# Performance work log

Hardware: AMD Instinct MI355X
Metric: run time of the kernel (lower is better)

## Reference

```python
import jax, jax.numpy as jnp
import numpy as np

BN_EPS = 1e-5


def setup_inputs() -> dict:
    key = jax.random.key(0)
    k1, k2 = jax.random.split(key)
    B, Cin, H, W_ = 16, 2048, 64, 64
    Cout = 256
    x = jax.random.normal(k1, (B, Cin, H, W_), dtype=jnp.float32)
    # 1x1 conv weight (bias-free, followed by BN) stored as [Cout, Cin]
    W = jax.random.normal(k2, (Cout, Cin), dtype=jnp.float32) * (1.0 / np.sqrt(Cin))
    gamma = jnp.ones((Cout,), dtype=jnp.float32)
    beta = jnp.zeros((Cout,), dtype=jnp.float32)
    running_mean = jnp.zeros((Cout,), dtype=jnp.float32)
    running_var = jnp.ones((Cout,), dtype=jnp.float32)
    return {"x": x, "W": W, "gamma": gamma, "beta": beta,
            "running_mean": running_mean, "running_var": running_var}


def reference(x, W, gamma, beta, running_mean, running_var):
    B, Cin, H, Wd = x.shape
    # Global average pool -> [B, Cin]
    pooled = jnp.mean(x, axis=(2, 3))
    # 1x1 conv on 1x1 spatial == GEMM: [B, Cin] @ [Cin, Cout] -> [B, Cout]
    y = jnp.einsum('bc,oc->bo', pooled, W)
    # BatchNorm2d in eval mode (running stats), fused scale/shift
    inv_std = jax.lax.rsqrt(running_var + BN_EPS)
    y = (y - running_mean) * (gamma * inv_std) + beta
    # ReLU
    y = jnp.maximum(y, 0.0)
    # Bilinear upsample from 1x1 (align_corners=False) == pure broadcast
    out = jnp.broadcast_to(y[:, :, None, None], (B, y.shape[1], H, Wd))
    return out
```

## Files before the change

kernel.cpp:

```cpp
#include <hip/hip_runtime.h>

#define BN_EPS 1e-5f

__global__ __launch_bounds__(256) void pool_kernel(const float* __restrict__ x,
                                                   float* __restrict__ pooled) {
    const int plane = blockIdx.x;
    const float4* xp = reinterpret_cast<const float4*>(x + (size_t)plane * 4096);
    float s = 0.f;
#pragma unroll
    for (int j = 0; j < 4; ++j) {
        float4 v = xp[threadIdx.x + j * 256];
        s += (v.x + v.y) + (v.z + v.w);
    }
#pragma unroll
    for (int off = 32; off > 0; off >>= 1) s += __shfl_down(s, off, 64);
    __shared__ float wsum[4];
    const int wid = threadIdx.x >> 6;
    const int lane = threadIdx.x & 63;
    if (lane == 0) wsum[wid] = s;
    __syncthreads();
    if (threadIdx.x == 0) {
        float t = (wsum[0] + wsum[1]) + (wsum[2] + wsum[3]);
        pooled[plane] = t * (1.0f / 4096.0f);
    }
}

__global__ __launch_bounds__(256) void gemm_bn_bcast_kernel(
    const float* __restrict__ pooled, const float* __restrict__ Wm,
    const float* __restrict__ gamma, const float* __restrict__ beta,
    const float* __restrict__ rmean, const float* __restrict__ rvar,
    float* __restrict__ out) {
    const int wid = threadIdx.x >> 6;
    const int lane = threadIdx.x & 63;
    const int gw = blockIdx.x * 4 + wid;
    const int b = gw >> 8;
    const int o = gw & 255;

    const float4* pr = reinterpret_cast<const float4*>(pooled + b * 2048);
    const float4* wr = reinterpret_cast<const float4*>(Wm + (size_t)o * 2048);
    float s = 0.f;
#pragma unroll
    for (int k = 0; k < 8; ++k) {
        float4 p = pr[lane + k * 64];
        float4 w = wr[lane + k * 64];
        s += p.x * w.x + p.y * w.y + p.z * w.z + p.w * w.w;
    }
#pragma unroll
    for (int off = 32; off > 0; off >>= 1) s += __shfl_down(s, off, 64);
    float y = __shfl(s, 0, 64);

    const float inv_std = rsqrtf(rvar[o] + BN_EPS);
    y = (y - rmean[o]) * (gamma[o] * inv_std) + beta[o];
    y = fmaxf(y, 0.f);

    float4 v = make_float4(y, y, y, y);
    float4* op = reinterpret_cast<float4*>(out + (size_t)gw * 4096);
#pragma unroll
    for (int j = 0; j < 16; ++j) op[j * 64 + lane] = v;
}

extern "C" void kernel_launch(void* const* d_in, const int* in_sizes, int n_in,
                              void* d_out, int out_size, void* d_ws, size_t ws_size,
                              hipStream_t stream) {
    const float* x     = (const float*)d_in[0];
    const float* Wm    = (const float*)d_in[1];
    const float* gamma = (const float*)d_in[2];
    const float* beta  = (const float*)d_in[3];
    const float* rmean = (const float*)d_in[4];
    const float* rvar  = (const float*)d_in[5];
    float* out = (float*)d_out;

    float* pooled = (float*)d_ws;

    pool_kernel<<<16 * 2048, 256, 0, stream>>>(x, pooled);
    gemm_bn_bcast_kernel<<<4096 / 4, 256, 0, stream>>>(pooled, Wm, gamma, beta,
                                                       rmean, rvar, out);
}
```

Baseline: 111.2 us.

## Fuse pool and GEMM into persistent cooperative kernel with grid sync

```diff
diff --git a/kernel.cpp b/kernel.cpp
--- a/kernel.cpp
+++ b/kernel.cpp
@@ -1,62 +1,92 @@
 #include <hip/hip_runtime.h>
+#include <hip/hip_cooperative_groups.h>
+
+namespace cg = cooperative_groups;
 
 #define BN_EPS 1e-5f
+#define NPLANES (16 * 2048)
+#define NOUT    (16 * 256)
 
-__global__ __launch_bounds__(256) void pool_kernel(const float* __restrict__ x,
-                                                   float* __restrict__ pooled) {
-    const int plane = blockIdx.x;
-    const float4* xp = reinterpret_cast<const float4*>(x + (size_t)plane * 4096);
+typedef float f32x4 __attribute__((ext_vector_type(4)));
+
+__device__ __forceinline__ void pool_plane(const float* __restrict__ x,
+                                           float* __restrict__ pooled,
+                                           int plane, int lane) {
+    const f32x4* xp = reinterpret_cast<const f32x4*>(x + (size_t)plane * 4096);
     float s = 0.f;
 #pragma unroll
-    for (int j = 0; j < 4; ++j) {
-        float4 v = xp[threadIdx.x + j * 256];
+    for (int k = 0; k < 16; ++k) {
+        f32x4 v = __builtin_nontemporal_load(&xp[lane + k * 64]);
         s += (v.x + v.y) + (v.z + v.w);
     }
 #pragma unroll
     for (int off = 32; off > 0; off >>= 1) s += __shfl_down(s, off, 64);
-    __shared__ float wsum[4];
-    const int wid = threadIdx.x >> 6;
-    const int lane = threadIdx.x & 63;
-    if (lane == 0) wsum[wid] = s;
-    __syncthreads();
-    if (threadIdx.x == 0) {
-        float t = (wsum[0] + wsum[1]) + (wsum[2] + wsum[3]);
-        pooled[plane] = t * (1.0f / 4096.0f);
-    }
+    if (lane == 0) pooled[plane] = s * (1.0f / 4096.0f);
 }
 
-__global__ __launch_bounds__(256) void gemm_bn_bcast_kernel(
-    const float* __restrict__ pooled, const float* __restrict__ Wm,
-    const float* __restrict__ gamma, const float* __restrict__ beta,
-    const float* __restrict__ rmean, const float* __restrict__ rvar,
-    float* __restrict__ out) {
-    const int wid = threadIdx.x >> 6;
-    const int lane = threadIdx.x & 63;
-    const int gw = blockIdx.x * 4 + wid;
-    const int b = gw >> 8;
-    const int o = gw & 255;
-
-    const float4* pr = reinterpret_cast<const float4*>(pooled + b * 2048);
-    const float4* wr = reinterpret_cast<const float4*>(Wm + (size_t)o * 2048);
+__device__ __forceinline__ void gemm_bn_bcast(
+    int idx, int lane, const float* __restrict__ pooled,
+    const float* __restrict__ Wm, const float* __restrict__ gamma,
+    const float* __restrict__ beta, const float* __restrict__ rmean,
+    const float* __restrict__ rvar, float* __restrict__ out) {
+    const int b = idx >> 8;
+    const int o = idx & 255;
+    const f32x4* pr = reinterpret_cast<const f32x4*>(pooled + b * 2048);
+    const f32x4* wr = reinterpret_cast<const f32x4*>(Wm + (size_t)o * 2048);
     float s = 0.f;
 #pragma unroll
     for (int k = 0; k < 8; ++k) {
-        float4 p = pr[lane + k * 64];
-        float4 w = wr[lane + k * 64];
+        f32x4 p = pr[lane + k * 64];
+        f32x4 w = wr[lane + k * 64];
         s += p.x * w.x + p.y * w.y + p.z * w.z + p.w * w.w;
     }
 #pragma unroll
     for (int off = 32; off > 0; off >>= 1) s += __shfl_down(s, off, 64);
     float y = __shfl(s, 0, 64);
+    y = (y - rmean[o]) * (gamma[o] * rsqrtf(rvar[o] + BN_EPS)) + beta[o];
+    y = fmaxf(y, 0.f);
+    f32x4 v = {y, y, y, y};
+    f32x4* op = reinterpret_cast<f32x4*>(out + (size_t)idx * 4096);
+#pragma unroll
+    for (int j = 0; j < 16; ++j)
+        __builtin_nontemporal_store(v, &op[j * 64 + lane]);
+}
 
-    const float inv_std = rsqrtf(rvar[o] + BN_EPS);
-    y = (y - rmean[o]) * (gamma[o] * inv_std) + beta[o];
-    y = fmaxf(y, 0.f);
+__global__ __launch_bounds__(256, 4) void fused_kernel(
+    const float* __restrict__ x, const float* __restrict__ Wm,
+    const float* __restrict__ gamma, const float* __restrict__ beta,
+    const float* __restrict__ rmean, const float* __restrict__ rvar,
+    float* __restrict__ pooled, float* __restrict__ out) {
+    const int lane = threadIdx.x & 63;
+    const int gw   = blockIdx.x * 4 + (threadIdx.x >> 6);
+    const int NW   = gridDim.x * 4;
 
-    float4 v = make_float4(y, y, y, y);
-    float4* op = reinterpret_cast<float4*>(out + (size_t)gw * 4096);
-#pragma unroll
-    for (int j = 0; j < 16; ++j) op[j * 64 + lane] = v;
+    for (int plane = gw; plane < NPLANES; plane += NW)
+        pool_plane(x, pooled, plane, lane);
+
+    __threadfence();
+    cg::this_grid().sync();
+    __threadfence();
+
+    for (int idx = gw; idx < NOUT; idx += NW)
+        gemm_bn_bcast(idx, lane, pooled, Wm, gamma, beta, rmean, rvar, out);
+}
+
+__global__ __launch_bounds__(256) void pool_kernel(const float* __restrict__ x,
+                                                   float* __restrict__ pooled) {
+    const int lane = threadIdx.x & 63;
+    const int gw   = blockIdx.x * 4 + (threadIdx.x >> 6);
+    pool_plane(x, pooled, gw, lane);
+}
+
+__global__ __launch_bounds__(256) void gemm_kernel(
+    const float* __restrict__ pooled, const float* __restrict__ Wm,
+    const float* __restrict__ gamma, const float* __restrict__ beta,
+    const float* __restrict__ rmean, const float* __restrict__ rvar,
+    float* __restrict__ out) {
+    const int lane = threadIdx.x & 63;
+    const int gw   = blockIdx.x * 4 + (threadIdx.x >> 6);
+    gemm_bn_bcast(gw, lane, pooled, Wm, gamma, beta, rmean, rvar, out);
 }
 
 extern "C" void kernel_launch(void* const* d_in, const int* in_sizes, int n_in,
@@ -68,11 +98,27 @@
     const float* beta  = (const float*)d_in[3];
     const float* rmean = (const float*)d_in[4];
     const float* rvar  = (const float*)d_in[5];
-    float* out = (float*)d_out;
-
+    float* out    = (float*)d_out;
     float* pooled = (float*)d_ws;
 
-    pool_kernel<<<16 * 2048, 256, 0, stream>>>(x, pooled);
-    gemm_bn_bcast_kernel<<<4096 / 4, 256, 0, stream>>>(pooled, Wm, gamma, beta,
-                                                       rmean, rvar, out);
+    int maxBlocksPerCU = 0;
+    hipError_t qerr = hipOccupancyMaxActiveBlocksPerMultiprocessor(
+        &maxBlocksPerCU, fused_kernel, 256, 0);
+
+    bool launched = false;
+    if (qerr == hipSuccess && maxBlocksPerCU > 0) {
+        int grid = maxBlocksPerCU * 256;
+        if (grid > 1024) grid = 1024;
+        void* args[] = {(void*)&x, (void*)&Wm, (void*)&gamma, (void*)&beta,
+                        (void*)&rmean, (void*)&rvar, (void*)&pooled, (void*)&out};
+        hipError_t lerr = hipLaunchCooperativeKernel(
+            fused_kernel, dim3(grid), dim3(256), args, 0, stream);
+        launched = (lerr == hipSuccess);
+    }
+
+    if (!launched) {
+        pool_kernel<<<NPLANES / 4, 256, 0, stream>>>(x, pooled);
+        gemm_kernel<<<NOUT / 4, 256, 0, stream>>>(pooled, Wm, gamma, beta,
+                                                  rmean, rvar, out);
+    }
 }
```

Result: slower. 367.1 us (+230.1%).
